# Kernel optimization log

Hardware: AMD Instinct MI355X
Metric: run time of the kernel (lower is better)

## Reference

```python
import jax, jax.numpy as jnp
import numpy as np

N, F_IN, F_OUT, N_HEAD = 4096, 256, 64, 4
EDGE_P = 0.01  # sparsity of the random adjacency


def setup_inputs() -> dict:
    key = jax.random.key(0)
    k_h, k_adj, k_w, k_as, k_ad = jax.random.split(key, 5)
    h = jax.random.normal(k_h, (N, F_IN), dtype=jnp.float32)
    # random boolean adjacency with self-loops so every softmax row is valid
    adj = jax.random.uniform(k_adj, (N, N)) < EDGE_P
    adj = adj | jnp.eye(N, dtype=bool)
    # xavier_uniform-style params
    lim_w = float(np.sqrt(6.0 / (F_IN + F_OUT)))
    lim_a = float(np.sqrt(6.0 / (F_OUT + 1)))
    w = jax.random.uniform(k_w, (N_HEAD, F_IN, F_OUT), minval=-lim_w, maxval=lim_w, dtype=jnp.float32)
    a_src = jax.random.uniform(k_as, (N_HEAD, F_OUT, 1), minval=-lim_a, maxval=lim_a, dtype=jnp.float32)
    a_dst = jax.random.uniform(k_ad, (N_HEAD, F_OUT, 1), minval=-lim_a, maxval=lim_a, dtype=jnp.float32)
    bias = jnp.zeros((F_OUT,), dtype=jnp.float32)
    return {"h": h, "adj": adj, "w": w, "a_src": a_src, "a_dst": a_dst, "bias": bias}


def reference(h, adj, w, a_src, a_dst, bias):
    # h_prime[k] = h @ w[k]  -> [H, n, f_out]
    h_prime = jnp.einsum('nf,hfo->hno', h, w)
    # attention logits: attn[k,i,j] = src[k,i] + dst[k,j]
    src = jnp.einsum('hno,ho->hn', h_prime, a_src[..., 0])  # [H, n]
    dst = jnp.einsum('hno,ho->hn', h_prime, a_dst[..., 0])  # [H, n]
    scores = src[:, :, None] + dst[:, None, :]              # [H, n, n]
    scores = jnp.where(scores >= 0, scores, 0.2 * scores)   # leaky_relu(0.2)
    neg = jnp.asarray(jnp.finfo(scores.dtype).min, scores.dtype)
    scores = jnp.where(adj[None, :, :], scores, neg)
    attn = jax.nn.softmax(scores, axis=-1)                  # [H, n, n]
    out = jnp.einsum('hij,hjo->iho', attn, h_prime)         # [n, H, f_out]
    return out + bias
```

## Files before the change

kernel.cpp:

```cpp
#include <hip/hip_runtime.h>

#define NN 4096
#define FIN 256
#define FOUT 64
#define NH 4
#define CAP 128
#define WROW 258

typedef __attribute__((ext_vector_type(8))) short bf16x8;
typedef __attribute__((ext_vector_type(4))) float f32x4;

__device__ __forceinline__ unsigned short f2bf(float f) {
    unsigned u = __float_as_uint(f);
    u = (u + 0x7fff + ((u >> 16) & 1)) >> 16;
    return (unsigned short)u;
}
__device__ __forceinline__ float bf2f(unsigned short s) {
    return __uint_as_float((unsigned)s << 16);
}

__global__ __launch_bounds__(256) void gat_scanbits(
    const int* __restrict__ adj, unsigned long long* __restrict__ bits)
{
    const int lane = threadIdx.x & 63;
    const int tid  = blockIdx.x * 256 + threadIdx.x;
    const int STR  = 2048 * 256;
#pragma unroll
    for (int it = 0; it < 4; ++it) {
        const int g0 = tid + (2 * it) * STR;
        const int g1 = g0 + STR;
        const int4 a0 = ((const int4*)adj)[g0];
        const int4 a1 = ((const int4*)adj)[g1];

        const unsigned long long x0 = __ballot(a0.x != 0);
        const unsigned long long y0 = __ballot(a0.y != 0);
        const unsigned long long z0 = __ballot(a0.z != 0);
        const unsigned long long w0 = __ballot(a0.w != 0);
        unsigned long long m0 = x0;
        m0 = ((lane & 3) == 1) ? y0 : m0;
        m0 = ((lane & 3) == 2) ? z0 : m0;
        m0 = ((lane & 3) == 3) ? w0 : m0;
        if (lane < 4)
            bits[(size_t)(g0 >> 10) * 64 + ((g0 >> 6) & 15) * 4 + lane] = m0;

        const unsigned long long x1 = __ballot(a1.x != 0);
        const unsigned long long y1 = __ballot(a1.y != 0);
        const unsigned long long z1 = __ballot(a1.z != 0);
        const unsigned long long w1 = __ballot(a1.w != 0);
        unsigned long long m1 = x1;
        m1 = ((lane & 3) == 1) ? y1 : m1;
        m1 = ((lane & 3) == 2) ? z1 : m1;
        m1 = ((lane & 3) == 3) ? w1 : m1;
        if (lane < 4)
            bits[(size_t)(g1 >> 10) * 64 + ((g1 >> 6) & 15) * 4 + lane] = m1;
    }
}

__global__ __launch_bounds__(256) void gat_hprime(
    const float* __restrict__ h, const float* __restrict__ w,
    const float* __restrict__ a_src, const float* __restrict__ a_dst,
    unsigned short* __restrict__ hb, float* __restrict__ sd)
{
    const int b = blockIdx.x, t = threadIdx.x;
    const int head = b & 3, n0 = (b >> 2) * 32;
    const int wv = t >> 6, lane = t & 63;
    const int lrow = lane & 15, lk8 = lane >> 4;

    __shared__ __align__(16) unsigned short ws[64 * WROW];
    __shared__ float sdbuf[2][2][16][2];

#pragma unroll
    for (int i = 0; i < 16; ++i) {
        const int k  = (t >> 4) + i * 16;
        const int o4 = (t & 15) * 4;
        const float4 v = *(const float4*)(w + ((size_t)head * FIN + k) * FOUT + o4);
        ws[(o4 + 0) * WROW + k] = f2bf(v.x);
        ws[(o4 + 1) * WROW + k] = f2bf(v.y);
        ws[(o4 + 2) * WROW + k] = f2bf(v.z);
        ws[(o4 + 3) * WROW + k] = f2bf(v.w);
    }

    const float* hrow = h + (size_t)(n0 + (wv >> 1) * 16 + lrow) * FIN + lk8 * 8;
    bf16x8 a[8];
#pragma unroll
    for (int ks = 0; ks < 8; ++ks) {
        const float4 v0 = *(const float4*)(hrow + ks * 32);
        const float4 v1 = *(const float4*)(hrow + ks * 32 + 4);
        union { bf16x8 v; unsigned short s[8]; } u;
        u.s[0] = f2bf(v0.x); u.s[1] = f2bf(v0.y);
        u.s[2] = f2bf(v0.z); u.s[3] = f2bf(v0.w);
        u.s[4] = f2bf(v1.x); u.s[5] = f2bf(v1.y);
        u.s[6] = f2bf(v1.z); u.s[7] = f2bf(v1.w);
        a[ks] = u.v;
    }
    __syncthreads();

    const int obase = (wv & 1) * 32;
    f32x4 acc[2] = {{0.f,0.f,0.f,0.f},{0.f,0.f,0.f,0.f}};
#pragma unroll
    for (int ks = 0; ks < 8; ++ks) {
#pragma unroll
        for (int nt = 0; nt < 2; ++nt) {
            const bf16x8 bf = *(const bf16x8*)
                &ws[(obase + nt * 16 + lrow) * WROW + ks * 32 + lk8 * 8];
            acc[nt] = __builtin_amdgcn_mfma_f32_16x16x32_bf16(a[ks], bf, acc[nt], 0, 0, 0);
        }
    }

    const int mbase = n0 + (wv >> 1) * 16 + lk8 * 4;
#pragma unroll
    for (int nt = 0; nt < 2; ++nt)
#pragma unroll
        for (int r = 0; r < 4; ++r)
            hb[((size_t)head * NN + mbase + r) * FOUT + obase + nt * 16 + lrow] =
                f2bf(acc[nt][r]);

    float as_nt[2], ad_nt[2];
#pragma unroll
    for (int nt = 0; nt < 2; ++nt) {
        as_nt[nt] = a_src[head * FOUT + obase + nt * 16 + lrow];
        ad_nt[nt] = a_dst[head * FOUT + obase + nt * 16 + lrow];
    }
    float psr[4] = {0.f,0.f,0.f,0.f}, pdr[4] = {0.f,0.f,0.f,0.f};
#pragma unroll
    for (int nt = 0; nt < 2; ++nt)
#pragma unroll
        for (int r = 0; r < 4; ++r) {
            psr[r] = fmaf(acc[nt][r], as_nt[nt], psr[r]);
            pdr[r] = fmaf(acc[nt][r], ad_nt[nt], pdr[r]);
        }
#pragma unroll
    for (int r = 0; r < 4; ++r)
#pragma unroll
        for (int off = 1; off <= 8; off <<= 1) {
            psr[r] += __shfl_xor(psr[r], off, 64);
            pdr[r] += __shfl_xor(pdr[r], off, 64);
        }
    if (lrow == 0)
#pragma unroll
        for (int r = 0; r < 4; ++r) {
            sdbuf[wv >> 1][wv & 1][lk8 * 4 + r][0] = psr[r];
            sdbuf[wv >> 1][wv & 1][lk8 * 4 + r][1] = pdr[r];
        }
    __syncthreads();
    if ((wv & 1) == 0 && lrow == 0) {
        const int p = wv >> 1;
#pragma unroll
        for (int r = 0; r < 4; ++r) {
            const int n = lk8 * 4 + r;
            const int node = n0 + p * 16 + n;
            sd[(size_t)node * 8 + head]     = sdbuf[p][0][n][0] + sdbuf[p][1][n][0];
            sd[(size_t)node * 8 + 4 + head] = sdbuf[p][0][n][1] + sdbuf[p][1][n][1];
        }
    }
}

__global__ __launch_bounds__(256) void gat_attn(
    const unsigned long long* __restrict__ bits,
    const unsigned short* __restrict__ hb, const float* __restrict__ sd,
    const float* __restrict__ bias, float* __restrict__ out)
{
    const int i = blockIdx.x, t = threadIdx.x, wv = t >> 6, lane = t & 63;

    __shared__ int   idx_l[CAP];
    __shared__ float sc[NH][CAP];
    __shared__ int   cnt;
    __shared__ float inv_sum[NH];

    if (wv == 0) {
        unsigned long long m = bits[(size_t)i * 64 + lane];
        const int c = __popcll(m);
        int pre = c;
#pragma unroll
        for (int off = 1; off < 64; off <<= 1) {
            const int nb = __shfl_up(pre, off, 64);
            if (lane >= off) pre += nb;
        }
        int p = pre - c;
        const int cb = (lane >> 2) * 256 + (lane & 3);
        while (m) {
            const int bpos = __ffsll((unsigned long long)m) - 1;
            if (p < CAP) idx_l[p] = cb + 4 * bpos;
            ++p;
            m &= m - 1;
        }
        if (lane == 63) cnt = pre;
    }
    __syncthreads();

    const int count = min(cnt, CAP);
    const int cpad  = (count + 7) & ~7;

    if (t < count) {
        const int j = idx_l[t];
        const float4 sv = *(const float4*)(sd + (size_t)i * 8);
        const float4 dv = *(const float4*)(sd + (size_t)j * 8 + 4);
        const float s0 = sv.x + dv.x, s1 = sv.y + dv.y;
        const float s2 = sv.z + dv.z, s3 = sv.w + dv.w;
        sc[0][t] = (s0 >= 0.f) ? s0 : 0.2f * s0;
        sc[1][t] = (s1 >= 0.f) ? s1 : 0.2f * s1;
        sc[2][t] = (s2 >= 0.f) ? s2 : 0.2f * s2;
        sc[3][t] = (s3 >= 0.f) ? s3 : 0.2f * s3;
    } else if (t < cpad) {
        idx_l[t] = 0;
#pragma unroll
        for (int hh = 0; hh < NH; ++hh) sc[hh][t] = 0.f;
    }
    __syncthreads();

    {
        float m = -3.4e38f;
        for (int p = lane; p < count; p += 64) m = fmaxf(m, sc[wv][p]);
#pragma unroll
        for (int off = 32; off >= 1; off >>= 1) m = fmaxf(m, __shfl_xor(m, off, 64));
        float e = 0.f;
        for (int p = lane; p < count; p += 64) {
            const float v = __expf(sc[wv][p] - m);
            sc[wv][p] = v;
            e += v;
        }
#pragma unroll
        for (int off = 32; off >= 1; off >>= 1) e += __shfl_xor(e, off, 64);
        if (lane == 0) inv_sum[wv] = 1.f / e;
    }
    __syncthreads();

    float accv = 0.f;
    const unsigned short* hp = hb + (size_t)(wv * NN) * FOUT + lane;
    for (int p0 = 0; p0 < cpad; p0 += 8) {
        int jj[8]; unsigned short vv[8]; float ww[8];
#pragma unroll
        for (int k = 0; k < 8; ++k) jj[k] = idx_l[p0 + k];
#pragma unroll
        for (int k = 0; k < 8; ++k) vv[k] = hp[(size_t)jj[k] * FOUT];
#pragma unroll
        for (int k = 0; k < 8; ++k) ww[k] = sc[wv][p0 + k];
#pragma unroll
        for (int k = 0; k < 8; ++k) accv = fmaf(ww[k], bf2f(vv[k]), accv);
    }
    out[(size_t)i * (NH * FOUT) + wv * FOUT + lane] = accv * inv_sum[wv] + bias[lane];
}

extern "C" void kernel_launch(void* const* d_in, const int* in_sizes, int n_in,
                              void* d_out, int out_size, void* d_ws, size_t ws_size,
                              hipStream_t stream) {
    const float* h     = (const float*)d_in[0];
    const int*   adj   = (const int*)d_in[1];
    const float* w     = (const float*)d_in[2];
    const float* a_src = (const float*)d_in[3];
    const float* a_dst = (const float*)d_in[4];
    const float* bias  = (const float*)d_in[5];
    float* out = (float*)d_out;

    unsigned short* hb = (unsigned short*)d_ws;
    float* sd          = (float*)(hb + (size_t)NH * NN * FOUT);
    unsigned long long* bits = (unsigned long long*)(sd + (size_t)NN * 8);

    gat_scanbits<<<2048, 256, 0, stream>>>(adj, bits);
    gat_hprime<<<512, 256, 0, stream>>>(h, w, a_src, a_dst, hb, sd);
    gat_attn<<<NN, 256, 0, stream>>>(bits, hb, sd, bias, out);
}
```

Baseline: 40.57 us.

## Fuse adjacency bit-packing and h' projection into one prep kernel

Merges the adjacency-scan kernel and the h' projection kernel into a single launch, with extra blocks doing the scan, so one kernel launch goes away and the two independent stages can run at the same time. The bit packing also changes from wave ballots to per-thread packing of 32 consecutive columns into a uint32, which gives a simpler row-major bitmask that the attention kernel decodes with two 32-bit words per lane. The scan blocks reserve the large shared-memory tile even though they do not use it, which may limit occupancy. Each thread now reads 128 contiguous bytes, so adjacent threads' loads no longer coalesce as cleanly.

```diff
diff --git a/kernel.cpp b/kernel.cpp
--- a/kernel.cpp
+++ b/kernel.cpp
@@ -6,6 +6,8 @@
 #define NH 4
 #define CAP 128
 #define WROW 258
+#define HPB 512
+#define SCB 2048
 
 typedef __attribute__((ext_vector_type(8))) short bf16x8;
 typedef __attribute__((ext_vector_type(4))) float f32x4;
@@ -19,55 +21,44 @@
     return __uint_as_float((unsigned)s << 16);
 }
 
-__global__ __launch_bounds__(256) void gat_scanbits(
-    const int* __restrict__ adj, unsigned long long* __restrict__ bits)
-{
-    const int lane = threadIdx.x & 63;
-    const int tid  = blockIdx.x * 256 + threadIdx.x;
-    const int STR  = 2048 * 256;
-#pragma unroll
-    for (int it = 0; it < 4; ++it) {
-        const int g0 = tid + (2 * it) * STR;
-        const int g1 = g0 + STR;
-        const int4 a0 = ((const int4*)adj)[g0];
-        const int4 a1 = ((const int4*)adj)[g1];
-
-        const unsigned long long x0 = __ballot(a0.x != 0);
-        const unsigned long long y0 = __ballot(a0.y != 0);
-        const unsigned long long z0 = __ballot(a0.z != 0);
-        const unsigned long long w0 = __ballot(a0.w != 0);
-        unsigned long long m0 = x0;
-        m0 = ((lane & 3) == 1) ? y0 : m0;
-        m0 = ((lane & 3) == 2) ? z0 : m0;
-        m0 = ((lane & 3) == 3) ? w0 : m0;
-        if (lane < 4)
-            bits[(size_t)(g0 >> 10) * 64 + ((g0 >> 6) & 15) * 4 + lane] = m0;
-
-        const unsigned long long x1 = __ballot(a1.x != 0);
-        const unsigned long long y1 = __ballot(a1.y != 0);
-        const unsigned long long z1 = __ballot(a1.z != 0);
-        const unsigned long long w1 = __ballot(a1.w != 0);
-        unsigned long long m1 = x1;
-        m1 = ((lane & 3) == 1) ? y1 : m1;
-        m1 = ((lane & 3) == 2) ? z1 : m1;
-        m1 = ((lane & 3) == 3) ? w1 : m1;
-        if (lane < 4)
-            bits[(size_t)(g1 >> 10) * 64 + ((g1 >> 6) & 15) * 4 + lane] = m1;
-    }
-}
-
-__global__ __launch_bounds__(256) void gat_hprime(
-    const float* __restrict__ h, const float* __restrict__ w,
-    const float* __restrict__ a_src, const float* __restrict__ a_dst,
-    unsigned short* __restrict__ hb, float* __restrict__ sd)
+__global__ __launch_bounds__(256) void gat_prep(
+    const float* __restrict__ h, const int* __restrict__ adj,
+    const float* __restrict__ w, const float* __restrict__ a_src,
+    const float* __restrict__ a_dst,
+    unsigned short* __restrict__ hb, float* __restrict__ sd,
+    unsigned int* __restrict__ bits32)
 {
     const int b = blockIdx.x, t = threadIdx.x;
-    const int head = b & 3, n0 = (b >> 2) * 32;
     const int wv = t >> 6, lane = t & 63;
-    const int lrow = lane & 15, lk8 = lane >> 4;
 
     __shared__ __align__(16) unsigned short ws[64 * WROW];
     __shared__ float sdbuf[2][2][16][2];
+
+    if (b >= HPB) {
+        const int sb   = b - HPB;
+        const int row  = sb * 2 + (wv >> 1);
+        const int half = wv & 1;
+        const int colbase = half * 2048 + lane * 32;
+        const int4* p = (const int4*)(adj + (size_t)row * NN + colbase);
+
+        int4 v[8];
+#pragma unroll
+        for (int it = 0; it < 8; ++it) v[it] = p[it];
+
+        unsigned u = 0;
+#pragma unroll
+        for (int it = 0; it < 8; ++it) {
+            u |= (v[it].x != 0 ? 1u : 0u) << (it * 4 + 0);
+            u |= (v[it].y != 0 ? 1u : 0u) << (it * 4 + 1);
+            u |= (v[it].z != 0 ? 1u : 0u) << (it * 4 + 2);
+            u |= (v[it].w != 0 ? 1u : 0u) << (it * 4 + 3);
+        }
+        bits32[(size_t)row * 128 + half * 64 + lane] = u;
+        return;
+    }
+
+    const int head = b & 3, n0 = (b >> 2) * 32;
+    const int lrow = lane & 15, lk8 = lane >> 4;
 
 #pragma unroll
     for (int i = 0; i < 16; ++i) {
@@ -156,7 +147,7 @@
 }
 
 __global__ __launch_bounds__(256) void gat_attn(
-    const unsigned long long* __restrict__ bits,
+    const unsigned int* __restrict__ bits32,
     const unsigned short* __restrict__ hb, const float* __restrict__ sd,
     const float* __restrict__ bias, float* __restrict__ out)
 {
@@ -168,8 +159,9 @@
     __shared__ float inv_sum[NH];
 
     if (wv == 0) {
-        unsigned long long m = bits[(size_t)i * 64 + lane];
-        const int c = __popcll(m);
+        unsigned w0 = bits32[(size_t)i * 128 + 2 * lane];
+        unsigned w1 = bits32[(size_t)i * 128 + 2 * lane + 1];
+        const int c = __popc(w0) + __popc(w1);
         int pre = c;
 #pragma unroll
         for (int off = 1; off < 64; off <<= 1) {
@@ -177,12 +169,18 @@
             if (lane >= off) pre += nb;
         }
         int p = pre - c;
-        const int cb = (lane >> 2) * 256 + (lane & 3);
-        while (m) {
-            const int bpos = __ffsll((unsigned long long)m) - 1;
-            if (p < CAP) idx_l[p] = cb + 4 * bpos;
+        const int base = lane * 64;
+        while (w0) {
+            const int bp = __ffs(w0) - 1;
+            if (p < CAP) idx_l[p] = base + bp;
             ++p;
-            m &= m - 1;
+            w0 &= w0 - 1;
+        }
+        while (w1) {
+            const int bp = __ffs(w1) - 1;
+            if (p < CAP) idx_l[p] = base + 32 + bp;
+            ++p;
+            w1 &= w1 - 1;
         }
         if (lane == 63) cnt = pre;
     }
@@ -254,9 +252,8 @@
 
     unsigned short* hb = (unsigned short*)d_ws;
     float* sd          = (float*)(hb + (size_t)NH * NN * FOUT);
-    unsigned long long* bits = (unsigned long long*)(sd + (size_t)NN * 8);
-
-    gat_scanbits<<<2048, 256, 0, stream>>>(adj, bits);
-    gat_hprime<<<512, 256, 0, stream>>>(h, w, a_src, a_dst, hb, sd);
-    gat_attn<<<NN, 256, 0, stream>>>(bits, hb, sd, bias, out);
-}
+    unsigned int* bits32 = (unsigned int*)(sd + (size_t)NN * 8);
+
+    gat_prep<<<HPB + SCB, 256, 0, stream>>>(h, adj, w, a_src, a_dst, hb, sd, bits32);
+    gat_attn<<<NN, 256, 0, stream>>>(bits32, hb, sd, bias, out);
+}
```

Result: faster. 38.92 us (-4.1%).
